# Performance work log

Hardware: AMD Instinct MI355X
Metric: run time of the kernel (lower is better)

Reference implementation:

```python
import jax, jax.numpy as jnp
import numpy as np

C = 1024
T = 2048
B = 8

def setup_inputs() -> dict:
    key = jax.random.key(0)
    ks = jax.random.split(key, 7)
    s = lambda fan_in: 1.0 / np.sqrt(fan_in)
    return {
        "x":     jax.random.normal(ks[0], (B, T, C), dtype=jnp.float32),
        "w_qkv": jax.random.uniform(ks[1], (C, 3 * C), jnp.float32, -s(C), s(C)),
        "w_proj": jax.random.uniform(ks[2], (C, C), jnp.float32, -s(C), s(C)),
        "w1":    jax.random.uniform(ks[3], (C, 2 * C), jnp.float32, -s(C), s(C)),
        "w2":    jax.random.uniform(ks[4], (2 * C, C), jnp.float32, -s(2 * C), s(2 * C)),
        "g1":    jnp.ones((C,), jnp.float32),
        "g2":    jnp.ones((C,), jnp.float32),
    }

def rmsnorm(x, g, eps=1e-6):
    return x * jax.lax.rsqrt(jnp.mean(x * x, axis=-1, keepdims=True) + eps) * g

def reference(x, w_qkv, w_proj, w1, w2, g1, g2):
    t = x.shape[1]
    # --- attention ---
    h = rmsnorm(x, g1)
    qkv = h @ w_qkv                               # [B,T,3C]
    q, k, v = jnp.split(qkv, 3, axis=-1)
    scores = jnp.einsum('bqc,bkc->bqk', q, k) * (C ** -0.5)  # [B,T,T]
    causal = jnp.triu(jnp.ones((t, t), dtype=bool), k=1)
    scores = jnp.where(causal, -jnp.inf, scores)
    attn = jax.nn.softmax(scores, axis=-1)
    x = x + (attn @ v) @ w_proj
    # --- ffn ---
    h = rmsnorm(x, g2)
    return x + (jax.nn.silu(h @ w1)) @ w2
```

## Files before the change

### kernel.cpp

```cpp
#include <hip/hip_runtime.h>
#include <hip/hip_bf16.h>
#include <stdint.h>


#define C_DIM 1024
#define T_DIM 2048
#define B_DIM 8

typedef float f32x4 __attribute__((ext_vector_type(4)));
typedef __bf16 bf16x8 __attribute__((ext_vector_type(8)));

typedef const __attribute__((address_space(1))) void gvoid_t;
typedef __attribute__((address_space(3))) void lvoid_t;

__device__ __forceinline__ void gload_lds16(const void* g, void* l) {
    __builtin_amdgcn_global_load_lds((gvoid_t*)g, (lvoid_t*)l, 16, 0, 0);
}

__device__ __forceinline__ unsigned short f2bf_bits(float f) {
    __hip_bfloat16 h = __float2bfloat16(f);
    return *reinterpret_cast<unsigned short*>(&h);
}

__device__ __forceinline__ void xcd_remap(int& bx, int& by, int& bz) {
    const int gx = gridDim.x, gy = gridDim.y;
    const int nwg = gx * gy * (int)gridDim.z;
    const int orig = bx + gx * (by + gy * bz);
    const int q = nwg >> 3, r = nwg & 7;
    const int xcd = orig & 7, pos = orig >> 3;
    const int neu = (xcd < r ? xcd * (q + 1) : r * (q + 1) + (xcd - r) * q) + pos;
    bx = neu % gx;
    const int t = neu / gx;
    by = t % gy;
    bz = t / gy;
}

#define BAR() do { __builtin_amdgcn_s_barrier(); __builtin_amdgcn_sched_barrier(0); } while(0)
#define VMCNT(n) do { asm volatile("s_waitcnt vmcnt(" #n ")" ::: "memory"); \
                      __builtin_amdgcn_sched_barrier(0); } while(0)
#define LGKM0() do { asm volatile("s_waitcnt lgkmcnt(0)" ::: "memory"); \
                     __builtin_amdgcn_sched_barrier(0); } while(0)

#define RD_A(dst, buf, hq) do { \
    _Pragma("unroll") \
    for (int mf_ = 0; mf_ < 4; ++mf_) { \
        const char* p_ = lds + (buf)*32768 + wrb + (hq)*8192 + mf_*2048; \
        dst[mf_][0] = *(const bf16x8*)(p_ + offk0); \
        dst[mf_][1] = *(const bf16x8*)(p_ + offk1); \
    } \
} while(0)

#define RD_B(dst, buf, nh) do { \
    _Pragma("unroll") \
    for (int n2_ = 0; n2_ < 2; ++n2_) { \
        const char* p_ = lds + 65536 + (buf)*32768 + wcb + ((nh)*2 + n2_)*2048; \
        dst[n2_][0] = *(const bf16x8*)(p_ + offk0); \
        dst[n2_][1] = *(const bf16x8*)(p_ + offk1); \
    } \
} while(0)

#define MMQ(aS, bS, Mh, Nh) do { \
    __builtin_amdgcn_s_setprio(1); \
    _Pragma("unroll") \
    for (int m4_ = 0; m4_ < 4; ++m4_) \
    _Pragma("unroll") \
    for (int n2_ = 0; n2_ < 2; ++n2_) \
    _Pragma("unroll") \
    for (int ks_ = 0; ks_ < 2; ++ks_) \
        acc[(Mh)*4 + m4_][(Nh)*2 + n2_] = __builtin_amdgcn_mfma_f32_16x16x32_bf16( \
            aS[m4_][ks_], bS[n2_][ks_], acc[(Mh)*4 + m4_][(Nh)*2 + n2_], 0, 0, 0); \
    __builtin_amdgcn_s_setprio(0); \
} while(0)

#define STA(buf, half, kt) do { \
    const int go_ = aoff + (half)*128*lda + (kt)*64; \
    char* lp_ = ldsw + (buf)*32768 + (half)*16384; \
    gload_lds16(A + go_,            lp_); \
    gload_lds16(A + go_ + 64*lda,   lp_ + 8192); \
} while(0)
#define STB(buf, half, kt) do { \
    const int go_ = boff + (half)*128*ldb + (kt)*64; \
    char* lp_ = ldsw + 65536 + (buf)*32768 + (half)*16384; \
    gload_lds16(Bt + go_,           lp_); \
    gload_lds16(Bt + go_ + 64*ldb,  lp_ + 8192); \
} while(0)

#define TILE_BODY(t, STG) do { \
    const int buf_ = (t) & 1; \
     \
    RD_B(bL, buf_, 0); \
    BAR(); LGKM0(); MMQ(aX, bL, 0, 0); BAR(); \
     \
    if (STG) STB(buf_, 0, (t) + 2); \
    RD_B(bH, buf_, 1); \
    BAR(); LGKM0(); MMQ(aX, bH, 0, 1); BAR(); \
     \
    if (STG) STB(buf_, 1, (t) + 2); \
    RD_A(aY, buf_, 1); \
    BAR(); LGKM0(); MMQ(aY, bH, 1, 1); \
    if (STG) { VMCNT(4); } else { VMCNT(0); } \
    BAR(); \
     \
    if (STG) { STA(buf_, 0, (t) + 2); STA(buf_, 1, (t) + 2); } \
    if ((t) + 1 < NT) RD_A(aX, buf_ ^ 1, 0); \
    BAR(); LGKM0(); MMQ(aY, bL, 1, 0); BAR(); \
} while(0)

template<int EPI, int CMODE>
__global__ __launch_bounds__(512, 2)
void gemm256(const __hip_bfloat16* A, const __hip_bfloat16* Bt,
             void* Cout, const float* R, void* C2, void* C3,
             int K, int lda, int ldb, int ldc,
             long long sA, long long sB, long long sC, float scale)
{
    int bx = blockIdx.x, by = blockIdx.y, bz = blockIdx.z;
    xcd_remap(bx, by, bz);
    if constexpr (CMODE == 1) { if (bx > by) return; }

    const int tid  = threadIdx.x;
    const int lane = tid & 63, wave = tid >> 6;
    const int l15  = lane & 15, l4 = lane >> 4;
    const int wr   = wave >> 2, wc = wave & 3;
    const int m0   = by * 256, n0 = bx * 256;
    const int z    = bz;

    A  += (long long)z * sA;
    Bt += (long long)z * sB;

    __shared__ __align__(16) char lds_[131072];
    char* lds  = lds_;
    char* ldsw = lds_ + wave * 1024;

    int kmax = K;
    if constexpr (CMODE == 2) { int km = m0 + 256; kmax = km < K ? km : K; }
    const int NT = kmax >> 6;

    const int offk0 = l15 * 128 + (((l4)     ^ (l15 & 7)) << 4);
    const int offk1 = l15 * 128 + (((4 + l4) ^ (l15 & 7)) << 4);
    const int wrb = wr * 16384, wcb = wc * 8192;

    const int rowq  = tid >> 3;
    const int sslot = (tid & 7) ^ (rowq & 7);
    const int aoff  = (m0 + rowq) * lda + sslot * 8;
    const int boff  = (n0 + rowq) * ldb + sslot * 8;

    f32x4 acc[8][4];
#pragma unroll
    for (int i = 0; i < 8; ++i)
#pragma unroll
        for (int j = 0; j < 4; ++j) acc[i][j] = (f32x4){0.f, 0.f, 0.f, 0.f};
    bf16x8 aX[4][2], aY[4][2], bL[2][2], bH[2][2];

    STB(0, 0, 0); STB(0, 1, 0); STA(0, 0, 0); STA(0, 1, 0);
    STB(1, 0, 1); STB(1, 1, 1); STA(1, 0, 1); STA(1, 1, 1);
    VMCNT(8);
    BAR();
    RD_A(aX, 0, 0);

    int t = 0;
    for (; t < NT - 2; ++t) TILE_BODY(t, true);
    for (; t < NT; ++t)     TILE_BODY(t, false);

    asm volatile("s_waitcnt vmcnt(0)" ::: "memory");

    const long long cbase = (long long)z * sC;
#pragma unroll
    for (int mf = 0; mf < 8; ++mf) {
        const int rbase = m0 + wr * 128 + mf * 16 + l4 * 4;
#pragma unroll
        for (int nf = 0; nf < 4; ++nf) {
            const int col = n0 + wc * 64 + nf * 16 + l15;
#pragma unroll
            for (int r = 0; r < 4; ++r) {
                const float v = acc[mf][nf][r];
                const int row = rbase + r;
                if constexpr (EPI == 6) {
                    const int seg = col >> 10, ncol = col & 1023;
                    if (seg == 0) {
                        ((__hip_bfloat16*)Cout)[(long long)row * 1024 + ncol] =
                            __float2bfloat16(v);
                    } else if (seg == 1) {
                        ((__hip_bfloat16*)C2)[(long long)row * 1024 + ncol] =
                            __float2bfloat16(v);
                    } else {
                        const int b = row >> 11, tt = row & 2047;
                        ((__hip_bfloat16*)C3)[((long long)b * C_DIM + ncol) * T_DIM + tt] =
                            __float2bfloat16(v);
                    }
                } else {
                    const long long idx = cbase + (long long)row * ldc + col;
                    if constexpr (EPI == 0) {
                        ((__hip_bfloat16*)Cout)[idx] = __float2bfloat16(v);
                    } else if constexpr (EPI == 2) {
                        ((float*)Cout)[idx] = v + R[idx];
                    } else if constexpr (EPI == 3) {
                        const float s = v / (1.f + __expf(-v));
                        ((__hip_bfloat16*)Cout)[idx] = __float2bfloat16(s);
                    } else {
                        ((__hip_bfloat16*)Cout)[idx] = __float2bfloat16(v * scale);
                    }
                }
            }
        }
    }
}

__global__ __launch_bounds__(256)
void rmsnorm_kernel(const float* __restrict__ x, const float* __restrict__ g,
                    __hip_bfloat16* __restrict__ out)
{
    const long long row = blockIdx.x;
    const int tid = threadIdx.x;
    const float4 v = ((const float4*)(x + row * C_DIM))[tid];
    float ss = v.x * v.x + v.y * v.y + v.z * v.z + v.w * v.w;
#pragma unroll
    for (int off = 32; off; off >>= 1) ss += __shfl_xor(ss, off);
    __shared__ float red[4];
    if ((tid & 63) == 0) red[tid >> 6] = ss;
    __syncthreads();
    ss = red[0] + red[1] + red[2] + red[3];
    const float sc = rsqrtf(ss * (1.0f / C_DIM) + 1e-6f);
    const float4 gv = ((const float4*)g)[tid];
    ushort4 u;
    u.x = f2bf_bits(v.x * sc * gv.x);
    u.y = f2bf_bits(v.y * sc * gv.y);
    u.z = f2bf_bits(v.z * sc * gv.z);
    u.w = f2bf_bits(v.w * sc * gv.w);
    *(ushort4*)(out + row * C_DIM + tid * 4) = u;
}

__global__ __launch_bounds__(256)
void softmax_causal(__hip_bfloat16* __restrict__ SP)
{
    const int i = blockIdx.x, b = blockIdx.y;
    __hip_bfloat16* row = SP + ((long long)b * T_DIM + i) * T_DIM;
    const int tid = threadIdx.x;
    const int jbase = tid * 8;

    uint4 raw = ((const uint4*)row)[tid];
    float v[8];
    const unsigned w[4] = {raw.x, raw.y, raw.z, raw.w};
#pragma unroll
    for (int c = 0; c < 4; ++c) {
        unsigned lo = w[c] << 16;
        unsigned hi = w[c] & 0xFFFF0000u;
        v[2 * c]     = __uint_as_float(lo);
        v[2 * c + 1] = __uint_as_float(hi);
    }
#pragma unroll
    for (int e = 0; e < 8; ++e)
        if (jbase + e > i) v[e] = -1e30f;

    float m = v[0];
#pragma unroll
    for (int e = 1; e < 8; ++e) m = fmaxf(m, v[e]);
#pragma unroll
    for (int off = 32; off; off >>= 1) m = fmaxf(m, __shfl_xor(m, off));
    __shared__ float redm[4], reds[4];
    if ((tid & 63) == 0) redm[tid >> 6] = m;
    __syncthreads();
    m = fmaxf(fmaxf(redm[0], redm[1]), fmaxf(redm[2], redm[3]));

    float e8[8];
    float s = 0.f;
#pragma unroll
    for (int e = 0; e < 8; ++e) { e8[e] = __expf(v[e] - m); s += e8[e]; }
#pragma unroll
    for (int off = 32; off; off >>= 1) s += __shfl_xor(s, off);
    if ((tid & 63) == 0) reds[tid >> 6] = s;
    __syncthreads();
    s = reds[0] + reds[1] + reds[2] + reds[3];
    const float inv = 1.f / s;

    uint4 outw;
    unsigned o[4];
#pragma unroll
    for (int c = 0; c < 4; ++c) {
        unsigned lo = f2bf_bits(e8[2 * c] * inv);
        unsigned hi = f2bf_bits(e8[2 * c + 1] * inv);
        o[c] = lo | (hi << 16);
    }
    outw.x = o[0]; outw.y = o[1]; outw.z = o[2]; outw.w = o[3];
    ((uint4*)row)[tid] = outw;
}

__global__ __launch_bounds__(256)
void wcast_t(const float* __restrict__ in, __hip_bfloat16* __restrict__ out,
             int K, int N)
{
    __shared__ float t[32][33];
    const int n0 = blockIdx.x * 32, k0 = blockIdx.y * 32;
    const int tx = threadIdx.x, ty = threadIdx.y;
#pragma unroll
    for (int r = ty; r < 32; r += 8)
        t[r][tx] = in[(long long)(k0 + r) * N + n0 + tx];
    __syncthreads();
#pragma unroll
    for (int r = ty; r < 32; r += 8)
        out[(long long)(n0 + r) * K + k0 + tx] = __float2bfloat16(t[tx][r]);
}

extern "C" void kernel_launch(void* const* d_in, const int* in_sizes, int n_in,
                              void* d_out, int out_size, void* d_ws, size_t ws_size,
                              hipStream_t stream)
{
    const float* x      = (const float*)d_in[0];
    const float* w_qkv  = (const float*)d_in[1];
    const float* w_proj = (const float*)d_in[2];
    const float* w1     = (const float*)d_in[3];
    const float* w2     = (const float*)d_in[4];
    const float* g1     = (const float*)d_in[5];
    const float* g2     = (const float*)d_in[6];
    float* out = (float*)d_out;
    char* ws = (char*)d_ws;

    const size_t SP_off = 0;
    const size_t h_off  = 0;
    const size_t u_off  = 0;
    const size_t q_off  = 67108864ull;
    const size_t k_off  = 100663296ull;
    const size_t vT_off = 134217728ull;
    const size_t wq_off = 167772160ull;
    const size_t wp_off = wq_off + 6291456ull;
    const size_t w1_off = wp_off + 2097152ull;
    const size_t w2_off = w1_off + 4194304ull;
    const size_t NEED   = w2_off + 4194304ull;

    if (ws_size < NEED) return;

    auto bf = [&](size_t off) { return (__hip_bfloat16*)(ws + off); };

    wcast_t<<<dim3(96, 32), dim3(32, 8), 0, stream>>>(w_qkv,  bf(wq_off), 1024, 3072);
    wcast_t<<<dim3(32, 32), dim3(32, 8), 0, stream>>>(w_proj, bf(wp_off), 1024, 1024);
    wcast_t<<<dim3(64, 32), dim3(32, 8), 0, stream>>>(w1,     bf(w1_off), 1024, 2048);
    wcast_t<<<dim3(32, 64), dim3(32, 8), 0, stream>>>(w2,     bf(w2_off), 2048, 1024);

    rmsnorm_kernel<<<16384, 256, 0, stream>>>(x, g1, bf(h_off));

    gemm256<6, 0><<<dim3(12, 64, 1), 512, 0, stream>>>(
        bf(h_off), bf(wq_off), bf(q_off), nullptr, bf(k_off), bf(vT_off),
        1024, 1024, 1024, 1024, 0, 0, 0, 1.f);

    gemm256<4, 1><<<dim3(8, 8, 8), 512, 0, stream>>>(
        bf(q_off), bf(k_off), bf(SP_off), nullptr, nullptr, nullptr,
        1024, 1024, 1024, 2048,
        (long long)T_DIM * C_DIM, (long long)T_DIM * C_DIM, (long long)T_DIM * T_DIM,
        0.03125f);

    softmax_causal<<<dim3(2048, 8), 256, 0, stream>>>(bf(SP_off));

    gemm256<0, 2><<<dim3(4, 8, 8), 512, 0, stream>>>(
        bf(SP_off), bf(vT_off), bf(k_off) , nullptr, nullptr, nullptr,
        2048, 2048, 2048, 1024,
        (long long)T_DIM * T_DIM, (long long)C_DIM * T_DIM, (long long)T_DIM * C_DIM,
        1.f);

    gemm256<2, 0><<<dim3(4, 64, 1), 512, 0, stream>>>(
        bf(k_off) , bf(wp_off), out, x, nullptr, nullptr,
        1024, 1024, 1024, 1024, 0, 0, 0, 1.f);

    rmsnorm_kernel<<<16384, 256, 0, stream>>>(out, g2, bf(q_off));

    gemm256<3, 0><<<dim3(8, 64, 1), 512, 0, stream>>>(
        bf(q_off), bf(w1_off), bf(u_off), nullptr, nullptr, nullptr,
        1024, 1024, 1024, 2048, 0, 0, 0, 1.f);

    gemm256<2, 0><<<dim3(4, 64, 1), 512, 0, stream>>>(
        bf(u_off), bf(w2_off), out, (const float*)out, nullptr, nullptr,
        2048, 2048, 2048, 1024, 0, 0, 0, 1.f);
}
```

Measured before the change: 596.2 us.

## Simplify GEMM main loop to load-all-then-compute with single barrier per tile

Replaces the four-phase interleaved LDS-read/MFMA schedule in the GEMM K-loop with a simpler one. Each tile now reads all A and B fragments, runs all MFMAs under raised priority, drains lgkm and vm counters, hits one barrier, then issues the global-to-LDS loads for tile t+2. The goal is fewer barriers and fewer scheduling fences per tile, and more freedom for the compiler to order instructions. In exchange it loses the fine overlap of LDS reads with MFMA work and waits for all outstanding global loads each iteration, which can expose memory latency.

```diff
diff --git a/kernel.cpp b/kernel.cpp
--- a/kernel.cpp
+++ b/kernel.cpp
@@ -35,12 +35,6 @@
     bz = t / gy;
 }
 
-#define BAR() do { __builtin_amdgcn_s_barrier(); __builtin_amdgcn_sched_barrier(0); } while(0)
-#define VMCNT(n) do { asm volatile("s_waitcnt vmcnt(" #n ")" ::: "memory"); \
-                      __builtin_amdgcn_sched_barrier(0); } while(0)
-#define LGKM0() do { asm volatile("s_waitcnt lgkmcnt(0)" ::: "memory"); \
-                     __builtin_amdgcn_sched_barrier(0); } while(0)
-
 #define RD_A(dst, buf, hq) do { \
     _Pragma("unroll") \
     for (int mf_ = 0; mf_ < 4; ++mf_) { \
@@ -60,7 +54,6 @@
 } while(0)
 
 #define MMQ(aS, bS, Mh, Nh) do { \
-    __builtin_amdgcn_s_setprio(1); \
     _Pragma("unroll") \
     for (int m4_ = 0; m4_ < 4; ++m4_) \
     _Pragma("unroll") \
@@ -69,7 +62,6 @@
     for (int ks_ = 0; ks_ < 2; ++ks_) \
         acc[(Mh)*4 + m4_][(Nh)*2 + n2_] = __builtin_amdgcn_mfma_f32_16x16x32_bf16( \
             aS[m4_][ks_], bS[n2_][ks_], acc[(Mh)*4 + m4_][(Nh)*2 + n2_], 0, 0, 0); \
-    __builtin_amdgcn_s_setprio(0); \
 } while(0)
 
 #define STA(buf, half, kt) do { \
@@ -87,23 +79,18 @@
 
 #define TILE_BODY(t, STG) do { \
     const int buf_ = (t) & 1; \
-     \
-    RD_B(bL, buf_, 0); \
-    BAR(); LGKM0(); MMQ(aX, bL, 0, 0); BAR(); \
-     \
-    if (STG) STB(buf_, 0, (t) + 2); \
-    RD_B(bH, buf_, 1); \
-    BAR(); LGKM0(); MMQ(aX, bH, 0, 1); BAR(); \
-     \
-    if (STG) STB(buf_, 1, (t) + 2); \
-    RD_A(aY, buf_, 1); \
-    BAR(); LGKM0(); MMQ(aY, bH, 1, 1); \
-    if (STG) { VMCNT(4); } else { VMCNT(0); } \
-    BAR(); \
-     \
-    if (STG) { STA(buf_, 0, (t) + 2); STA(buf_, 1, (t) + 2); } \
-    if ((t) + 1 < NT) RD_A(aX, buf_ ^ 1, 0); \
-    BAR(); LGKM0(); MMQ(aY, bL, 1, 0); BAR(); \
+    bf16x8 a0[4][2], a1[4][2], b0v[2][2], b1v[2][2]; \
+    RD_A(a0, buf_, 0); RD_A(a1, buf_, 1); \
+    RD_B(b0v, buf_, 0); RD_B(b1v, buf_, 1); \
+    __builtin_amdgcn_s_setprio(1); \
+    MMQ(a0, b0v, 0, 0); MMQ(a0, b1v, 0, 1); \
+    MMQ(a1, b0v, 1, 0); MMQ(a1, b1v, 1, 1); \
+    __builtin_amdgcn_s_setprio(0); \
+    asm volatile("s_waitcnt lgkmcnt(0)" ::: "memory"); \
+    asm volatile("s_waitcnt vmcnt(0)" ::: "memory"); \
+    __builtin_amdgcn_s_barrier(); \
+    if (STG) { STB(buf_,0,(t)+2); STB(buf_,1,(t)+2); \
+               STA(buf_,0,(t)+2); STA(buf_,1,(t)+2); } \
 } while(0)
 
 template<int EPI, int CMODE>
@@ -149,13 +136,11 @@
     for (int i = 0; i < 8; ++i)
 #pragma unroll
         for (int j = 0; j < 4; ++j) acc[i][j] = (f32x4){0.f, 0.f, 0.f, 0.f};
-    bf16x8 aX[4][2], aY[4][2], bL[2][2], bH[2][2];
 
     STB(0, 0, 0); STB(0, 1, 0); STA(0, 0, 0); STA(0, 1, 0);
     STB(1, 0, 1); STB(1, 1, 1); STA(1, 0, 1); STA(1, 1, 1);
-    VMCNT(8);
-    BAR();
-    RD_A(aX, 0, 0);
+    asm volatile("s_waitcnt vmcnt(8)" ::: "memory");
+    __builtin_amdgcn_s_barrier();
 
     int t = 0;
     for (; t < NT - 2; ++t) TILE_BODY(t, true);
```

After: 583.5 us. 2.1% less time.
